# Kernel optimization log

Measured on AMD Instinct MI355X. Metric: run time of the kernel, lower is better.

## Reference

```python
import jax, jax.numpy as jnp
import numpy as np

H = 768   # hidden_dim * SMPL_NR_JOINTS = 32 * 24
O = 72    # output_dim * SMPL_NR_JOINTS = 3 * 24
B = 256
T = 100   # max_len (tgt.size(1))
SRC_LEN = 16


def setup_inputs() -> dict:
    key = jax.random.key(0)
    ks = jax.random.split(key, 10)
    s = 1.0 / np.sqrt(H)
    return {
        "src": jax.random.normal(ks[0], (B, SRC_LEN, H), jnp.float32),
        "tgt": jax.random.normal(ks[1], (B, T, O), jnp.float32),
        "h0": jax.random.normal(ks[2], (B, H), jnp.float32),
        "c0": jax.random.normal(ks[3], (B, H), jnp.float32),
        "W_ih": jax.random.uniform(ks[4], (4 * H, H), jnp.float32, -s, s),
        "W_hh": jax.random.uniform(ks[5], (4 * H, H), jnp.float32, -s, s),
        "b_ih": jax.random.uniform(ks[6], (4 * H,), jnp.float32, -s, s),
        "b_hh": jax.random.uniform(ks[7], (4 * H,), jnp.float32, -s, s),
        "W_post": jax.random.uniform(ks[8], (O, H), jnp.float32, -s, s),
        "b_post": jax.random.uniform(ks[9], (O,), jnp.float32, -s, s),
    }


def reference(src, tgt, h0, c0, W_ih, W_hh, b_ih, b_hh, W_post, b_post):
    max_len = tgt.shape[1]
    bias = b_ih + b_hh  # [4H]

    def step(carry, _):
        x, h, c = carry  # each [B, H]
        gates = x @ W_ih.T + h @ W_hh.T + bias  # [B, 4H]
        i, f, g, o = jnp.split(gates, 4, axis=-1)  # PyTorch gate order i,f,g,o
        c = jax.nn.sigmoid(f) * c + jax.nn.sigmoid(i) * jnp.tanh(g)
        h = jax.nn.sigmoid(o) * jnp.tanh(c)
        return (h, h, c), h  # decoder output feeds back as next input

    x0 = src[:, -1]  # out = src[:, -1].unsqueeze(1)
    _, outs = jax.lax.scan(step, (x0, h0, c0), None, length=max_len)  # [T, B, H]
    outs = jnp.transpose(outs, (1, 0, 2))  # [B, T, H]
    return outs @ W_post.T + b_post  # [B, T, O]
```

## Files before the change

### kernel.cpp

```cpp
#include <hip/hip_runtime.h>
#include <hip/hip_bf16.h>
#include <math.h>

#define H 768
#define B 256
#define T 100

typedef __attribute__((ext_vector_type(8))) short short8;
typedef __attribute__((ext_vector_type(4))) float f32x4;
typedef unsigned long long u64;

static __device__ __forceinline__ float sigm(float x) {
    return 1.0f / (1.0f + __expf(-x));
}
static __device__ __forceinline__ float tanh_fast(float x) {
    return 1.0f - 2.0f / (__expf(2.0f * x) + 1.0f);
}

__global__ void prep_all(const float* __restrict__ src, const float* __restrict__ h0,
                         const float* __restrict__ Wih, const float* __restrict__ Whh,
                         const float* __restrict__ bih, const float* __restrict__ bhh,
                         const float* __restrict__ Wpost,
                         __hip_bfloat16* __restrict__ Wc,
                         __hip_bfloat16* __restrict__ Wcat,
                         float* __restrict__ bias,
                         __hip_bfloat16* __restrict__ Wp,
                         __hip_bfloat16* __restrict__ A0,
                         u64* __restrict__ sig64)
{
    const int bx = blockIdx.x;
    const int y  = blockIdx.y;
    const int k  = bx * 256 + threadIdx.x;
    if (y < 3072) {
        float a = Wih[y * H + k];
        float b = Whh[y * H + k];
        Wc[y * H + k] = __float2bfloat16(a + b);
        Wcat[y * 1536 + k] = __float2bfloat16(a);
        Wcat[y * 1536 + H + k] = __float2bfloat16(b);
        if (bx == 0 && threadIdx.x == 0) bias[y] = bih[y] + bhh[y];
    } else if (y < 3152) {
        int r = y - 3072;
        Wp[r * H + k] = (r < 72) ? __float2bfloat16(Wpost[r * H + k])
                                 : __float2bfloat16(0.0f);
    } else if (y < 3408) {
        int b = y - 3152;
        A0[b * 1536 + k] = __float2bfloat16(src[(b * 16 + 15) * H + k]);
        A0[b * 1536 + H + k] = __float2bfloat16(h0[b * H + k]);
    } else {
        sig64[(size_t)(y - 3408) * 768 + k] = 0ull;
    }
}

#define LDS_H_STRIDE  772
#define LDS_T0_STRIDE 1540
#define XCH_STRIDE    17

#define LDW8(n0,n1,n2,n3,n4,n5,n6,n7, p) \
    asm volatile("global_load_dwordx4 %0, %8, off\n\t" \
                 "global_load_dwordx4 %1, %8, off offset:64\n\t" \
                 "global_load_dwordx4 %2, %8, off offset:128\n\t" \
                 "global_load_dwordx4 %3, %8, off offset:192\n\t" \
                 "global_load_dwordx4 %4, %8, off offset:256\n\t" \
                 "global_load_dwordx4 %5, %8, off offset:320\n\t" \
                 "global_load_dwordx4 %6, %8, off offset:384\n\t" \
                 "global_load_dwordx4 %7, %8, off offset:448\n\t" \
                 "s_waitcnt vmcnt(0)" \
                 : "=&v"(n0),"=&v"(n1),"=&v"(n2),"=&v"(n3), \
                   "=&v"(n4),"=&v"(n5),"=&v"(n6),"=&v"(n7) \
                 : "v"(p))

#define KSTEP(nm, idx) { \
    short8 a_ = *(const short8*)(&lds_h[col * LDS_H_STRIDE + (idx) * 32 + quad * 8]); \
    acc = __builtin_amdgcn_mfma_f32_16x16x32_bf16(a_, nm, acc, 0, 0, 0); }

static __device__ __forceinline__ bool sig_ok(u64 x) {
    return (unsigned short)x && (unsigned short)(x >> 16) &&
           (unsigned short)(x >> 32) && (unsigned short)(x >> 48);
}

__global__ __launch_bounds__(768, 3) void lstm_persist(
    const __hip_bfloat16* __restrict__ Wc,
    const __hip_bfloat16* __restrict__ Wcat,
    const float* __restrict__ bias,
    const float* __restrict__ c0in,
    const __hip_bfloat16* __restrict__ A0,
    unsigned* sig)
{
    const int mtg  = blockIdx.x >> 4;
    const int jg   = blockIdx.x & 15;
    const int tid  = threadIdx.x;
    const int lane = tid & 63;
    const int wave = tid >> 6;
    const int col  = lane & 15;
    const int quad = lane >> 4;
    const int jt_l = wave >> 2;
    const int gate = wave & 3;
    const int j    = jg * 48 + jt_l * 16 + col;

    __shared__ short lds_h[16 * LDS_T0_STRIDE];
    __shared__ float xch[12 * 16 * XCH_STRIDE];

    const short* wptr = (const short*)Wc + (size_t)(gate * H + j) * H + quad * 8;
    short8 w00,w01,w02,w03,w04,w05,w06,w07,w08,w09,w10,w11,
           w12,w13,w14,w15,w16,w17,w18,w19,w20,w21,w22,w23;
    LDW8(w00,w01,w02,w03,w04,w05,w06,w07, wptr);
    LDW8(w08,w09,w10,w11,w12,w13,w14,w15, wptr + 256);
    LDW8(w16,w17,w18,w19,w20,w21,w22,w23, wptr + 512);

    const int p    = tid;
    const int bb   = p / 24;
    const int jp   = p % 24;
    const int jloc = jp * 2;
    const int cjt  = jloc >> 4;
    const int jcol = jloc & 15;
    const int bglob = mtg * 16 + bb;
    const int jglob = jg * 48 + jloc;
    float c0v = 0.f, c1v = 0.f;
    float bi0=0,bi1=0,bf0=0,bf1=0,bg0=0,bg1=0,bo0=0,bo1=0;
    if (p < 384) {
        c0v = c0in[(size_t)bglob * H + jglob];
        c1v = c0in[(size_t)bglob * H + jglob + 1];
        bi0 = bias[0*H + jglob]; bi1 = bias[0*H + jglob + 1];
        bf0 = bias[1*H + jglob]; bf1 = bias[1*H + jglob + 1];
        bg0 = bias[2*H + jglob]; bg1 = bias[2*H + jglob + 1];
        bo0 = bias[3*H + jglob]; bo1 = bias[3*H + jglob + 1];
    }

    const u64* sig64c = (const u64*)sig;
    const int r0  = tid / 192;
    const int wrd = tid % 192;

    for (int t = 0; t < T; ++t) {
        f32x4 acc = {0.f, 0.f, 0.f, 0.f};

        if (t == 0) {
            const u64* a8 = (const u64*)((const short*)A0 + (size_t)(mtg * 16) * 1536);
#pragma unroll
            for (int i = 0; i < 8; ++i) {
                int idx = tid + i * 768;
                int br  = idx / 384;
                int ch  = idx % 384;
                *(u64*)&lds_h[br * LDS_T0_STRIDE + ch * 4] = a8[(size_t)br * 384 + ch];
            }
            __syncthreads();

            const short* wq = (const short*)Wcat + (size_t)(gate * H + j) * 1536 + quad * 8;
            for (int kk = 0; kk < 48; ++kk) {
                short8 a_ = *(const short8*)(&lds_h[col * LDS_T0_STRIDE + kk * 32 + quad * 8]);
                short8 b_ = *(const short8*)(wq + kk * 32);
                acc = __builtin_amdgcn_mfma_f32_16x16x32_bf16(a_, b_, acc, 0, 0, 0);
            }
        } else {
            const u64* hb = sig64c + ((size_t)(t - 1) * B + (size_t)(mtg * 16)) * 192 + wrd;
            u64 x0 = __hip_atomic_load(hb + (size_t)(r0     ) * 192,
                                       __ATOMIC_RELAXED, __HIP_MEMORY_SCOPE_AGENT);
            u64 x1 = __hip_atomic_load(hb + (size_t)(r0 +  4) * 192,
                                       __ATOMIC_RELAXED, __HIP_MEMORY_SCOPE_AGENT);
            u64 x2 = __hip_atomic_load(hb + (size_t)(r0 +  8) * 192,
                                       __ATOMIC_RELAXED, __HIP_MEMORY_SCOPE_AGENT);
            u64 x3 = __hip_atomic_load(hb + (size_t)(r0 + 12) * 192,
                                       __ATOMIC_RELAXED, __HIP_MEMORY_SCOPE_AGENT);
            unsigned pending = 0xFu;
            if (sig_ok(x0)) { *(u64*)&lds_h[(r0     ) * LDS_H_STRIDE + wrd * 4] = ~x0; pending &= ~1u; }
            if (sig_ok(x1)) { *(u64*)&lds_h[(r0 +  4) * LDS_H_STRIDE + wrd * 4] = ~x1; pending &= ~2u; }
            if (sig_ok(x2)) { *(u64*)&lds_h[(r0 +  8) * LDS_H_STRIDE + wrd * 4] = ~x2; pending &= ~4u; }
            if (sig_ok(x3)) { *(u64*)&lds_h[(r0 + 12) * LDS_H_STRIDE + wrd * 4] = ~x3; pending &= ~8u; }
            int guard = 0;
            while (pending && ++guard < (1 << 22)) {
                __builtin_amdgcn_s_sleep(4);
                if (pending & 1u) x0 = __hip_atomic_load(hb + (size_t)(r0     ) * 192,
                                        __ATOMIC_RELAXED, __HIP_MEMORY_SCOPE_AGENT);
                if (pending & 2u) x1 = __hip_atomic_load(hb + (size_t)(r0 +  4) * 192,
                                        __ATOMIC_RELAXED, __HIP_MEMORY_SCOPE_AGENT);
                if (pending & 4u) x2 = __hip_atomic_load(hb + (size_t)(r0 +  8) * 192,
                                        __ATOMIC_RELAXED, __HIP_MEMORY_SCOPE_AGENT);
                if (pending & 8u) x3 = __hip_atomic_load(hb + (size_t)(r0 + 12) * 192,
                                        __ATOMIC_RELAXED, __HIP_MEMORY_SCOPE_AGENT);
                if ((pending & 1u) && sig_ok(x0)) { *(u64*)&lds_h[(r0     ) * LDS_H_STRIDE + wrd * 4] = ~x0; pending &= ~1u; }
                if ((pending & 2u) && sig_ok(x1)) { *(u64*)&lds_h[(r0 +  4) * LDS_H_STRIDE + wrd * 4] = ~x1; pending &= ~2u; }
                if ((pending & 4u) && sig_ok(x2)) { *(u64*)&lds_h[(r0 +  8) * LDS_H_STRIDE + wrd * 4] = ~x2; pending &= ~4u; }
                if ((pending & 8u) && sig_ok(x3)) { *(u64*)&lds_h[(r0 + 12) * LDS_H_STRIDE + wrd * 4] = ~x3; pending &= ~8u; }
            }
            __syncthreads();

            KSTEP(w00,0)  KSTEP(w01,1)  KSTEP(w02,2)  KSTEP(w03,3)
            KSTEP(w04,4)  KSTEP(w05,5)  KSTEP(w06,6)  KSTEP(w07,7)
            KSTEP(w08,8)  KSTEP(w09,9)  KSTEP(w10,10) KSTEP(w11,11)
            KSTEP(w12,12) KSTEP(w13,13) KSTEP(w14,14) KSTEP(w15,15)
            KSTEP(w16,16) KSTEP(w17,17) KSTEP(w18,18) KSTEP(w19,19)
            KSTEP(w20,20) KSTEP(w21,21) KSTEP(w22,22) KSTEP(w23,23)
        }

        float* xw = &xch[(size_t)wave * 16 * XCH_STRIDE];
#pragma unroll
        for (int r = 0; r < 4; ++r)
            xw[(quad * 4 + r) * XCH_STRIDE + col] = acc[r];
        __syncthreads();

        if (p < 384) {
            const float* xg = &xch[(size_t)(cjt * 4) * 16 * XCH_STRIDE + bb * XCH_STRIDE + jcol];
            const int gs = 16 * XCH_STRIDE;
            float i0 = xg[0*gs] + bi0, i1 = xg[0*gs + 1] + bi1;
            float f0 = xg[1*gs] + bf0, f1 = xg[1*gs + 1] + bf1;
            float g0 = xg[2*gs] + bg0, g1 = xg[2*gs + 1] + bg1;
            float o0 = xg[3*gs] + bo0, o1 = xg[3*gs + 1] + bo1;
            float cn0 = sigm(f0) * c0v + sigm(i0) * tanh_fast(g0);
            float cn1 = sigm(f1) * c1v + sigm(i1) * tanh_fast(g1);
            c0v = cn0; c1v = cn1;
            __hip_bfloat16 h0b = __float2bfloat16(sigm(o0) * tanh_fast(cn0));
            __hip_bfloat16 h1b = __float2bfloat16(sigm(o1) * tanh_fast(cn1));
            unsigned lo = (unsigned)(unsigned short)~(*(unsigned short*)&h0b);
            unsigned hi = (unsigned)(unsigned short)~(*(unsigned short*)&h1b);
            __hip_atomic_store(&sig[((size_t)t * B + bglob) * 384 + (jglob >> 1)],
                               lo | (hi << 16),
                               __ATOMIC_RELAXED, __HIP_MEMORY_SCOPE_AGENT);
        }
        __syncthreads();
    }
}

__global__ __launch_bounds__(64) void proj(
    const short* __restrict__ Hs,
    const __hip_bfloat16* __restrict__ Wp,
    const float* __restrict__ bpost,
    float* __restrict__ out)
{
    const int mt = blockIdx.x;
    const int lane = threadIdx.x;
    const int col = lane & 15;
    const int quad = lane >> 4;

    const short* Ap = Hs + (size_t)(mt * 16 + col) * H + quad * 8;
    const short* Wb = (const short*)Wp;

    f32x4 acc[5];
#pragma unroll
    for (int nt = 0; nt < 5; ++nt) acc[nt] = (f32x4){0.f, 0.f, 0.f, 0.f};

    for (int k = 0; k < H; k += 32) {
        short8 a = ~(*(const short8*)(Ap + k));
#pragma unroll
        for (int nt = 0; nt < 5; ++nt) {
            short8 b = *(const short8*)(Wb + (size_t)(nt * 16 + col) * H + quad * 8 + k);
            acc[nt] = __builtin_amdgcn_mfma_f32_16x16x32_bf16(a, b, acc[nt], 0, 0, 0);
        }
    }

#pragma unroll
    for (int nt = 0; nt < 5; ++nt) {
        const int o = nt * 16 + col;
        if (o < 72) {
            const float bb = bpost[o];
#pragma unroll
            for (int r = 0; r < 4; ++r) {
                const int m = mt * 16 + quad * 4 + r;
                const int t = m >> 8;
                const int b = m & 255;
                out[((size_t)b * T + t) * 72 + o] = acc[nt][r] + bb;
            }
        }
    }
}


extern "C" void kernel_launch(void* const* d_in, const int* in_sizes, int n_in,
                              void* d_out, int out_size, void* d_ws, size_t ws_size,
                              hipStream_t stream) {
    const float* src   = (const float*)d_in[0];
    const float* h0    = (const float*)d_in[2];
    const float* c0    = (const float*)d_in[3];
    const float* Wih   = (const float*)d_in[4];
    const float* Whh   = (const float*)d_in[5];
    const float* bih   = (const float*)d_in[6];
    const float* bhh   = (const float*)d_in[7];
    const float* Wpost = (const float*)d_in[8];
    const float* bpost = (const float*)d_in[9];
    float* out = (float*)d_out;

    char* ws = (char*)d_ws;
    __hip_bfloat16* Wcat = (__hip_bfloat16*)(ws + 0);
    __hip_bfloat16* Wc   = (__hip_bfloat16*)(ws + 9437184);
    float*          bias = (float*)(ws + 14155776);
    __hip_bfloat16* Wp   = (__hip_bfloat16*)(ws + 14168064);
    __hip_bfloat16* A0   = (__hip_bfloat16*)(ws + 14290944);
    unsigned*       sig  = (unsigned*)(ws + 15863808);

    prep_all<<<dim3(3, 9808), 256, 0, stream>>>(src, h0, Wih, Whh, bih, bhh, Wpost,
                                                Wc, Wcat, bias, Wp, A0, (u64*)sig);

    lstm_persist<<<256, 768, 0, stream>>>(Wc, Wcat, bias, c0, A0, sig);

    proj<<<1600, 64, 0, stream>>>((const short*)sig, Wp, bpost, out);
}
```

Measured before the change: 460.5 us.

## Fuse weight prep into persistent LSTM kernel via cooperative launch

Removes the separate prep kernel that converted weights to bf16 and zeroed the signal buffer. The persistent kernel now reads fp32 weights directly, converts and sums them in registers, builds the initial input tile in LDS, zeroes its own slice of the signal buffer and converts W_post, then does a grid-wide sync before the recurrence. The step-0 matmul converts fp32 weights on the fly, and the sleep in the spin-wait loop is removed. This saves one launch and a large round trip of bf16 weight writes and reads, at the cost of a cooperative-launch grid barrier and extra fp32 traffic at startup.

```diff
diff --git a/kernel.cpp b/kernel.cpp
--- a/kernel.cpp
+++ b/kernel.cpp
@@ -1,4 +1,5 @@
 #include <hip/hip_runtime.h>
+#include <hip/hip_cooperative_groups.h>
 #include <hip/hip_bf16.h>
 #include <math.h>
 
@@ -8,7 +9,10 @@
 
 typedef __attribute__((ext_vector_type(8))) short short8;
 typedef __attribute__((ext_vector_type(4))) float f32x4;
+typedef __attribute__((ext_vector_type(4))) unsigned short us4;
 typedef unsigned long long u64;
+
+namespace cg = cooperative_groups;
 
 static __device__ __forceinline__ float sigm(float x) {
     return 1.0f / (1.0f + __expf(-x));
@@ -16,59 +20,36 @@
 static __device__ __forceinline__ float tanh_fast(float x) {
     return 1.0f - 2.0f / (__expf(2.0f * x) + 1.0f);
 }
-
-__global__ void prep_all(const float* __restrict__ src, const float* __restrict__ h0,
-                         const float* __restrict__ Wih, const float* __restrict__ Whh,
-                         const float* __restrict__ bih, const float* __restrict__ bhh,
-                         const float* __restrict__ Wpost,
-                         __hip_bfloat16* __restrict__ Wc,
-                         __hip_bfloat16* __restrict__ Wcat,
-                         float* __restrict__ bias,
-                         __hip_bfloat16* __restrict__ Wp,
-                         __hip_bfloat16* __restrict__ A0,
-                         u64* __restrict__ sig64)
-{
-    const int bx = blockIdx.x;
-    const int y  = blockIdx.y;
-    const int k  = bx * 256 + threadIdx.x;
-    if (y < 3072) {
-        float a = Wih[y * H + k];
-        float b = Whh[y * H + k];
-        Wc[y * H + k] = __float2bfloat16(a + b);
-        Wcat[y * 1536 + k] = __float2bfloat16(a);
-        Wcat[y * 1536 + H + k] = __float2bfloat16(b);
-        if (bx == 0 && threadIdx.x == 0) bias[y] = bih[y] + bhh[y];
-    } else if (y < 3152) {
-        int r = y - 3072;
-        Wp[r * H + k] = (r < 72) ? __float2bfloat16(Wpost[r * H + k])
-                                 : __float2bfloat16(0.0f);
-    } else if (y < 3408) {
-        int b = y - 3152;
-        A0[b * 1536 + k] = __float2bfloat16(src[(b * 16 + 15) * H + k]);
-        A0[b * 1536 + H + k] = __float2bfloat16(h0[b * H + k]);
-    } else {
-        sig64[(size_t)(y - 3408) * 768 + k] = 0ull;
-    }
+static __device__ __forceinline__ unsigned short bf16b(float x) {
+    __hip_bfloat16 h = __float2bfloat16(x);
+    return *(unsigned short*)&h;
+}
+static __device__ __forceinline__ short8 cvt8sum(const float* pa, const float* pb) {
+    f32x4 a0 = *(const f32x4*)pa, a1 = *(const f32x4*)(pa + 4);
+    f32x4 b0 = *(const f32x4*)pb, b1 = *(const f32x4*)(pb + 4);
+    short8 r;
+#pragma unroll
+    for (int e = 0; e < 4; ++e) {
+        r[e]     = (short)bf16b(a0[e] + b0[e]);
+        r[4 + e] = (short)bf16b(a1[e] + b1[e]);
+    }
+    return r;
+}
+static __device__ __forceinline__ short8 cvt8(const float* p) {
+    f32x4 a0 = *(const f32x4*)p, a1 = *(const f32x4*)(p + 4);
+    short8 r;
+#pragma unroll
+    for (int e = 0; e < 4; ++e) {
+        r[e]     = (short)bf16b(a0[e]);
+        r[4 + e] = (short)bf16b(a1[e]);
+    }
+    return r;
 }
 
 #define LDS_H_STRIDE  772
 #define LDS_T0_STRIDE 1540
 #define XCH_STRIDE    17
 
-#define LDW8(n0,n1,n2,n3,n4,n5,n6,n7, p) \
-    asm volatile("global_load_dwordx4 %0, %8, off\n\t" \
-                 "global_load_dwordx4 %1, %8, off offset:64\n\t" \
-                 "global_load_dwordx4 %2, %8, off offset:128\n\t" \
-                 "global_load_dwordx4 %3, %8, off offset:192\n\t" \
-                 "global_load_dwordx4 %4, %8, off offset:256\n\t" \
-                 "global_load_dwordx4 %5, %8, off offset:320\n\t" \
-                 "global_load_dwordx4 %6, %8, off offset:384\n\t" \
-                 "global_load_dwordx4 %7, %8, off offset:448\n\t" \
-                 "s_waitcnt vmcnt(0)" \
-                 : "=&v"(n0),"=&v"(n1),"=&v"(n2),"=&v"(n3), \
-                   "=&v"(n4),"=&v"(n5),"=&v"(n6),"=&v"(n7) \
-                 : "v"(p))
-
 #define KSTEP(nm, idx) { \
     short8 a_ = *(const short8*)(&lds_h[col * LDS_H_STRIDE + (idx) * 32 + quad * 8]); \
     acc = __builtin_amdgcn_mfma_f32_16x16x32_bf16(a_, nm, acc, 0, 0, 0); }
@@ -79,11 +60,15 @@
 }
 
 __global__ __launch_bounds__(768, 3) void lstm_persist(
-    const __hip_bfloat16* __restrict__ Wc,
-    const __hip_bfloat16* __restrict__ Wcat,
-    const float* __restrict__ bias,
+    const float* __restrict__ src,
+    const float* __restrict__ h0f,
     const float* __restrict__ c0in,
-    const __hip_bfloat16* __restrict__ A0,
+    const float* __restrict__ Wih,
+    const float* __restrict__ Whh,
+    const float* __restrict__ bih,
+    const float* __restrict__ bhh,
+    const float* __restrict__ Wpost,
+    __hip_bfloat16* __restrict__ Wp,
     unsigned* sig)
 {
     const int mtg  = blockIdx.x >> 4;
@@ -100,12 +85,53 @@
     __shared__ short lds_h[16 * LDS_T0_STRIDE];
     __shared__ float xch[12 * 16 * XCH_STRIDE];
 
-    const short* wptr = (const short*)Wc + (size_t)(gate * H + j) * H + quad * 8;
-    short8 w00,w01,w02,w03,w04,w05,w06,w07,w08,w09,w10,w11,
-           w12,w13,w14,w15,w16,w17,w18,w19,w20,w21,w22,w23;
-    LDW8(w00,w01,w02,w03,w04,w05,w06,w07, wptr);
-    LDW8(w08,w09,w10,w11,w12,w13,w14,w15, wptr + 256);
-    LDW8(w16,w17,w18,w19,w20,w21,w22,w23, wptr + 512);
+    u64* myz = (u64*)sig + (size_t)blockIdx.x * 19200 + tid;
+#pragma unroll
+    for (int k = 0; k < 25; ++k)
+        __hip_atomic_store(myz + (size_t)k * 768, 0ull,
+                           __ATOMIC_RELAXED, __HIP_MEMORY_SCOPE_AGENT);
+
+    if (blockIdx.x < 80 && tid < 192) {
+        const int r = blockIdx.x, k4 = tid * 4;
+        us4 w = (us4){0, 0, 0, 0};
+        if (r < 72) {
+            f32x4 v = *(const f32x4*)(Wpost + (size_t)r * H + k4);
+#pragma unroll
+            for (int e = 0; e < 4; ++e) w[e] = bf16b(v[e]);
+        }
+        *(us4*)((unsigned short*)Wp + (size_t)r * H + k4) = w;
+    }
+
+    const float* wi = Wih + (size_t)(gate * H + j) * H + quad * 8;
+    const float* wh = Whh + (size_t)(gate * H + j) * H + quad * 8;
+    short8 w00 = cvt8sum(wi +   0, wh +   0), w01 = cvt8sum(wi +  32, wh +  32),
+           w02 = cvt8sum(wi +  64, wh +  64), w03 = cvt8sum(wi +  96, wh +  96),
+           w04 = cvt8sum(wi + 128, wh + 128), w05 = cvt8sum(wi + 160, wh + 160),
+           w06 = cvt8sum(wi + 192, wh + 192), w07 = cvt8sum(wi + 224, wh + 224),
+           w08 = cvt8sum(wi + 256, wh + 256), w09 = cvt8sum(wi + 288, wh + 288),
+           w10 = cvt8sum(wi + 320, wh + 320), w11 = cvt8sum(wi + 352, wh + 352),
+           w12 = cvt8sum(wi + 384, wh + 384), w13 = cvt8sum(wi + 416, wh + 416),
+           w14 = cvt8sum(wi + 448, wh + 448), w15 = cvt8sum(wi + 480, wh + 480),
+           w16 = cvt8sum(wi + 512, wh + 512), w17 = cvt8sum(wi + 544, wh + 544),
+           w18 = cvt8sum(wi + 576, wh + 576), w19 = cvt8sum(wi + 608, wh + 608),
+           w20 = cvt8sum(wi + 640, wh + 640), w21 = cvt8sum(wi + 672, wh + 672),
+           w22 = cvt8sum(wi + 704, wh + 704), w23 = cvt8sum(wi + 736, wh + 736);
+
+#pragma unroll
+    for (int i = 0; i < 8; ++i) {
+        int idx = tid + i * 768;
+        int br  = idx / 384;
+        int ch  = idx % 384;
+        int cv  = ch * 4;
+        const float* pf = (cv < 768)
+            ? src + ((size_t)(mtg * 16 + br) * 16 + 15) * H + cv
+            : h0f + (size_t)(mtg * 16 + br) * H + (cv - 768);
+        f32x4 v = *(const f32x4*)pf;
+        us4 u;
+#pragma unroll
+        for (int e = 0; e < 4; ++e) u[e] = bf16b(v[e]);
+        *(us4*)&lds_h[br * LDS_T0_STRIDE + ch * 4] = u;
+    }
 
     const int p    = tid;
     const int bb   = p / 24;
@@ -120,11 +146,18 @@
     if (p < 384) {
         c0v = c0in[(size_t)bglob * H + jglob];
         c1v = c0in[(size_t)bglob * H + jglob + 1];
-        bi0 = bias[0*H + jglob]; bi1 = bias[0*H + jglob + 1];
-        bf0 = bias[1*H + jglob]; bf1 = bias[1*H + jglob + 1];
-        bg0 = bias[2*H + jglob]; bg1 = bias[2*H + jglob + 1];
-        bo0 = bias[3*H + jglob]; bo1 = bias[3*H + jglob + 1];
-    }
+        bi0 = bih[0*H + jglob]     + bhh[0*H + jglob];
+        bi1 = bih[0*H + jglob + 1] + bhh[0*H + jglob + 1];
+        bf0 = bih[1*H + jglob]     + bhh[1*H + jglob];
+        bf1 = bih[1*H + jglob + 1] + bhh[1*H + jglob + 1];
+        bg0 = bih[2*H + jglob]     + bhh[2*H + jglob];
+        bg1 = bih[2*H + jglob + 1] + bhh[2*H + jglob + 1];
+        bo0 = bih[3*H + jglob]     + bhh[3*H + jglob];
+        bo1 = bih[3*H + jglob + 1] + bhh[3*H + jglob + 1];
+    }
+
+    asm volatile("s_waitcnt vmcnt(0)" ::: "memory");
+    cg::this_grid().sync();
 
     const u64* sig64c = (const u64*)sig;
     const int r0  = tid / 192;
@@ -134,20 +167,16 @@
         f32x4 acc = {0.f, 0.f, 0.f, 0.f};
 
         if (t == 0) {
-            const u64* a8 = (const u64*)((const short*)A0 + (size_t)(mtg * 16) * 1536);
-#pragma unroll
-            for (int i = 0; i < 8; ++i) {
-                int idx = tid + i * 768;
-                int br  = idx / 384;
-                int ch  = idx % 384;
-                *(u64*)&lds_h[br * LDS_T0_STRIDE + ch * 4] = a8[(size_t)br * 384 + ch];
+            const float* qi = Wih + (size_t)(gate * H + j) * H + quad * 8;
+            const float* qh = Whh + (size_t)(gate * H + j) * H + quad * 8;
+            for (int kk = 0; kk < 24; ++kk) {
+                short8 a_ = *(const short8*)(&lds_h[col * LDS_T0_STRIDE + kk * 32 + quad * 8]);
+                short8 b_ = cvt8(qi + kk * 32);
+                acc = __builtin_amdgcn_mfma_f32_16x16x32_bf16(a_, b_, acc, 0, 0, 0);
             }
-            __syncthreads();
-
-            const short* wq = (const short*)Wcat + (size_t)(gate * H + j) * 1536 + quad * 8;
-            for (int kk = 0; kk < 48; ++kk) {
-                short8 a_ = *(const short8*)(&lds_h[col * LDS_T0_STRIDE + kk * 32 + quad * 8]);
-                short8 b_ = *(const short8*)(wq + kk * 32);
+            for (int kk = 0; kk < 24; ++kk) {
+                short8 a_ = *(const short8*)(&lds_h[col * LDS_T0_STRIDE + (24 + kk) * 32 + quad * 8]);
+                short8 b_ = cvt8(qh + kk * 32);
                 acc = __builtin_amdgcn_mfma_f32_16x16x32_bf16(a_, b_, acc, 0, 0, 0);
             }
         } else {
@@ -167,7 +196,6 @@
             if (sig_ok(x3)) { *(u64*)&lds_h[(r0 + 12) * LDS_H_STRIDE + wrd * 4] = ~x3; pending &= ~8u; }
             int guard = 0;
             while (pending && ++guard < (1 << 22)) {
-                __builtin_amdgcn_s_sleep(4);
                 if (pending & 1u) x0 = __hip_atomic_load(hb + (size_t)(r0     ) * 192,
                                         __ATOMIC_RELAXED, __HIP_MEMORY_SCOPE_AGENT);
                 if (pending & 2u) x1 = __hip_atomic_load(hb + (size_t)(r0 +  4) * 192,
@@ -278,17 +306,13 @@
     float* out = (float*)d_out;
 
     char* ws = (char*)d_ws;
-    __hip_bfloat16* Wcat = (__hip_bfloat16*)(ws + 0);
-    __hip_bfloat16* Wc   = (__hip_bfloat16*)(ws + 9437184);
-    float*          bias = (float*)(ws + 14155776);
-    __hip_bfloat16* Wp   = (__hip_bfloat16*)(ws + 14168064);
-    __hip_bfloat16* A0   = (__hip_bfloat16*)(ws + 14290944);
-    unsigned*       sig  = (unsigned*)(ws + 15863808);
-
-    prep_all<<<dim3(3, 9808), 256, 0, stream>>>(src, h0, Wih, Whh, bih, bhh, Wpost,
-                                                Wc, Wcat, bias, Wp, A0, (u64*)sig);
-
-    lstm_persist<<<256, 768, 0, stream>>>(Wc, Wcat, bias, c0, A0, sig);
+    __hip_bfloat16* Wp  = (__hip_bfloat16*)(ws + 14168064);
+    unsigned*       sig = (unsigned*)(ws + 15863808);
+
+    void* args[] = { (void*)&src, (void*)&h0, (void*)&c0, (void*)&Wih, (void*)&Whh,
+                     (void*)&bih, (void*)&bhh, (void*)&Wpost, (void*)&Wp, (void*)&sig };
+    hipLaunchCooperativeKernel((void*)lstm_persist, dim3(256), dim3(768),
+                               args, 0, stream);
 
     proj<<<1600, 64, 0, stream>>>((const short*)sig, Wp, bpost, out);
 }
```

Result: slower. 693.4 us (+50.6%).
